# Optimization experiments

Measured on AMD Instinct MI355X. Metric: run time of the kernel, lower is better.

The kernel has to match this reference:

```python
import jax, jax.numpy as jnp
import numpy as np

LEVEL_SIZES = [256, 128, 64, 32, 16]  # FPN map sizes for a 1024x1024 image
B, N, C = 16, 64, 8
EPS = 1e-8


def setup_inputs() -> dict:
    key = jax.random.key(0)
    ks = jax.random.split(key, 9)
    inp = {}
    for l, s in enumerate(LEVEL_SIZES):
        # attention maps must be in (0,1) for binary_cross_entropy
        inp[f"attn{l}"] = jax.random.uniform(ks[l], (B, C, s, s), jnp.float32, 1e-4, 1.0 - 1e-4)
    # boxes: x1,y1 in-image; widths/heights in [8, 512] px so all levels get boxes
    x1 = jax.random.uniform(ks[5], (B, N)) * (1024.0 - 16.0)
    y1 = jax.random.uniform(ks[6], (B, N)) * (1024.0 - 16.0)
    dw = 8.0 + jax.random.uniform(ks[7], (B, N)) * 504.0
    dh = 8.0 + jax.random.uniform(ks[8], (B, N)) * 504.0
    x2 = jnp.minimum(x1 + dw, 1024.0)
    y2 = jnp.minimum(y1 + dh, 1024.0)
    inp["bboxs"] = jnp.stack([x1, y1, x2, y2], axis=-1)  # [B, N, 4]
    inp["img_h"] = 1024
    inp["img_w"] = 1024
    inp["alpha"] = 5
    inp["beta"] = 2
    return inp


def reference(attn0, attn1, attn2, attn3, attn4, bboxs, img_h, img_w, alpha, beta):
    attns = [attn0, attn1, attn2, attn3, attn4]
    h = float(img_h)
    w = float(img_w)
    x1, y1, x2, y2 = bboxs[..., 0], bboxs[..., 1], bboxs[..., 2], bboxs[..., 3]  # each [B, N]
    # original validity filter: coords <= image bounds
    valid = (x1 <= w) & (y1 <= h) & (x2 <= w) & (y2 <= h)  # [B, N]
    area = jnp.abs((x2 - x1) * (y2 - y1))  # [B, N]

    per_level = []  # list of [B, C] losses
    for l, a in enumerate(attns):
        _, _, Hl, Wl = a.shape
        side = 2.0 ** (l + alpha)
        min_a = side ** 2
        max_a = (side * beta) ** 2
        sel = valid & (area >= min_a) & (area <= max_a)  # [B, N]

        sx = Wl / w
        sy = Hl / h
        # integer pixel bounds: int() truncation == floor for nonneg coords, then clamp
        xi1 = jnp.maximum(jnp.floor(x1 * sx), 0.0)
        yi1 = jnp.maximum(jnp.floor(y1 * sy), 0.0)
        xi2 = jnp.minimum(jnp.ceil(x2 * sx) + 1.0, float(Wl))
        yi2 = jnp.minimum(jnp.ceil(y2 * sy) + 1.0, float(Hl))

        ys = jnp.arange(Hl, dtype=jnp.float32)
        xs = jnp.arange(Wl, dtype=jnp.float32)
        # separable per-box row/col indicators; fold the level selector into rows
        row = ((ys[None, None, :] >= yi1[..., None]) & (ys[None, None, :] < yi2[..., None])
               & sel[..., None]).astype(jnp.float32)  # [B, N, Hl]
        col = ((xs[None, None, :] >= xi1[..., None]) & (xs[None, None, :] < xi2[..., None])
               ).astype(jnp.float32)  # [B, N, Wl]
        # OR over boxes == (sum of outer products) > 0
        mask_gt = (jnp.einsum('bnh,bnw->bhw', row, col) > 0).astype(jnp.float32)  # [B, Hl, Wl]

        t = mask_gt[:, None, :, :]  # broadcast over channels
        p = a  # [B, C, Hl, Wl]
        bce = jnp.mean(-(t * jnp.log(p) + (1.0 - t) * jnp.log(1.0 - p)), axis=(2, 3))  # [B, C]
        inter = 2.0 * jnp.sum(p * t, axis=(2, 3)) + EPS
        union = jnp.sum(p, axis=(2, 3)) + jnp.sum(t, axis=(2, 3)) + EPS
        dice = 1.0 - inter / union  # [B, C]
        per_level.append(0.5 * bce + 0.5 * dice)

    losses = jnp.stack(per_level, axis=1)  # [B, L, C]
    per_image = losses.mean(axis=(1, 2))  # [B]
    has_box = valid.any(axis=1)
    per_image = jnp.where(has_box, per_image, 0.0)
    return per_image.mean(keepdims=True)  # shape [1]
```

## Files before the change

kernel.cpp:

```cpp
#include <hip/hip_runtime.h>
#include <cstdint>

#define NBOX 64
#define NB   16
#define NC   8


__device__ __forceinline__ unsigned long long range_mask(int a, int e, int base) {
    int lo = a - base; lo = lo < 0 ? 0 : (lo > 64 ? 64 : lo);
    int hi = e - base; hi = hi < 0 ? 0 : (hi > 64 ? 64 : hi);
    if (hi <= lo) return 0ULL;
    unsigned long long hm = (hi >= 64) ? ~0ULL : ((1ULL << hi) - 1ULL);
    unsigned long long lm = (1ULL << lo) - 1ULL;
    return hm & ~lm;
}

__global__ __launch_bounds__(256)
void k_mask(const float* __restrict__ bboxs,
            const int* __restrict__ ih_p, const int* __restrict__ iw_p,
            const int* __restrict__ alpha_p, const int* __restrict__ beta_p,
            unsigned long long* __restrict__ mask,
            float* __restrict__ tcnt) {
    const int bid = blockIdx.x;
    const int l = bid % 5, b = bid / 5;
    const int Hl = 256 >> l;
    const int W64 = (Hl >= 64) ? (Hl >> 6) : 1;
    const int mb_[5] = {0, 16384, 20480, 21504, 22016};
    const int mbase = mb_[l] + b * Hl * W64;

    const float w = (float)iw_p[0], h = (float)ih_p[0];
    const int alpha = alpha_p[0], beta = beta_p[0];
    const float side = (float)(1 << (l + alpha));
    const float min_a = side * side;
    const float sb = side * (float)beta;
    const float max_a = sb * sb;
    const float sx = (float)Hl / w;
    const float sy = (float)Hl / h;

    __shared__ int rx1[NBOX], rx2[NBOX], ry1[NBOX], ry2[NBOX];
    const int tid = threadIdx.x;
    if (tid < NBOX) {
        const float* bb = bboxs + (size_t)(b * NBOX + tid) * 4;
        float x1 = bb[0], y1 = bb[1], x2 = bb[2], y2 = bb[3];
        bool valid = (x1 <= w) && (y1 <= h) && (x2 <= w) && (y2 <= h);
        float area = fabsf((x2 - x1) * (y2 - y1));
        bool sel = valid && (area >= min_a) && (area <= max_a);
        int xi1 = (int)fmaxf(floorf(x1 * sx), 0.f);
        int yi1 = (int)fmaxf(floorf(y1 * sy), 0.f);
        int xi2 = (int)fminf(ceilf(x2 * sx) + 1.f, (float)Hl);
        int yi2 = (int)fminf(ceilf(y2 * sy) + 1.f, (float)Hl);
        rx1[tid] = xi1; rx2[tid] = xi2;
        ry1[tid] = sel ? yi1 : 0;
        ry2[tid] = sel ? yi2 : 0;
    }
    __syncthreads();

    int myt = 0;
    for (int hh = tid; hh < Hl; hh += 256) {
        unsigned long long m0 = 0, m1 = 0, m2 = 0, m3 = 0;
        for (int n = 0; n < NBOX; ++n) {
            if (hh >= ry1[n] && hh < ry2[n]) {
                int a = rx1[n], e = rx2[n];
                m0 |= range_mask(a, e, 0);
                m1 |= range_mask(a, e, 64);
                m2 |= range_mask(a, e, 128);
                m3 |= range_mask(a, e, 192);
            }
        }
        unsigned long long* dst = mask + mbase + hh * W64;
        dst[0] = m0;              myt += __popcll(m0);
        if (W64 > 1) { dst[1] = m1; myt += __popcll(m1); }
        if (W64 > 2) { dst[2] = m2; myt += __popcll(m2);
                       dst[3] = m3; myt += __popcll(m3); }
    }

    for (int off = 32; off > 0; off >>= 1) myt += __shfl_down(myt, off, 64);
    __shared__ int red[4];
    if ((tid & 63) == 0) red[tid >> 6] = myt;
    __syncthreads();
    if (tid == 0)
        tcnt[l * NB + b] = (float)(red[0] + red[1] + red[2] + red[3]);
}

__global__ __launch_bounds__(256)
void k_sums(const float* __restrict__ a0, const float* __restrict__ a1,
            const float* __restrict__ a2, const float* __restrict__ a3,
            const float* __restrict__ a4,
            const unsigned long long* __restrict__ mask,
            float* __restrict__ acc) {
    const int bid = blockIdx.x;
    int l, rel;
    if      (bid < 1024) { l = 0; rel = bid; }
    else if (bid < 1280) { l = 1; rel = bid - 1024; }
    else if (bid < 1408) { l = 2; rel = bid - 1280; }
    else if (bid < 1536) { l = 3; rel = bid - 1408; }
    else                 { l = 4; rel = bid - 1536; }
    const int ntl[5] = {8, 2, 1, 1, 1};
    const int mb_[5] = {0, 16384, 20480, 21504, 22016};
    const int nt = ntl[l];
    const int tile = rel % nt;
    const int bc = rel / nt;
    const int c = bc & 7, b = bc >> 3;
    const int Hl = 256 >> l;
    const int P  = Hl * Hl;
    const int logW = 8 - l;
    const int W64 = (Hl >= 64) ? (Hl >> 6) : 1;

    const float* attn = (l == 0) ? a0 : (l == 1) ? a1 : (l == 2) ? a2 : (l == 3) ? a3 : a4;
    const float* p = attn + (size_t)(b * NC + c) * P;
    const unsigned long long* mrow = mask + mb_[l] + b * Hl * W64;

    const int start = tile * 8192;
    const int end = min(start + 8192, P);

    float bce = 0.f, ps = 0.f, pts = 0.f;
    const int tid = threadIdx.x;
    for (int i = start + tid * 4; i < end; i += 1024) {
        float4 v = *(const float4*)(p + i);
        int hh = i >> logW;
        int ww = i & (Hl - 1);
        unsigned long long wd = mrow[hh * W64 + (ww >> 6)];
        unsigned int bits = (unsigned int)(wd >> (ww & 63)) & 0xFu;
        { float pv = v.x; bool t = bits & 1u; bce -= __logf(t ? pv : 1.f - pv); ps += pv; if (t) pts += pv; }
        { float pv = v.y; bool t = bits & 2u; bce -= __logf(t ? pv : 1.f - pv); ps += pv; if (t) pts += pv; }
        { float pv = v.z; bool t = bits & 4u; bce -= __logf(t ? pv : 1.f - pv); ps += pv; if (t) pts += pv; }
        { float pv = v.w; bool t = bits & 8u; bce -= __logf(t ? pv : 1.f - pv); ps += pv; if (t) pts += pv; }
    }

    for (int off = 32; off > 0; off >>= 1) {
        bce += __shfl_down(bce, off, 64);
        ps  += __shfl_down(ps,  off, 64);
        pts += __shfl_down(pts, off, 64);
    }
    __shared__ float red[4][3];
    if ((tid & 63) == 0) {
        int wv = tid >> 6;
        red[wv][0] = bce; red[wv][1] = ps; red[wv][2] = pts;
    }
    __syncthreads();
    if (tid == 0) {
        float rb = red[0][0] + red[1][0] + red[2][0] + red[3][0];
        float rp = red[0][1] + red[1][1] + red[2][1] + red[3][1];
        float rt = red[0][2] + red[1][2] + red[2][2] + red[3][2];
        float* dst = acc + ((size_t)(l * NB + b) * NC + c) * 3;
        atomicAdd(dst + 0, rb);
        atomicAdd(dst + 1, rp);
        atomicAdd(dst + 2, rt);
    }
}

__global__ void k_final(const float* __restrict__ acc, const float* __restrict__ tcnt,
                        const float* __restrict__ bboxs,
                        const int* __restrict__ ih_p, const int* __restrict__ iw_p,
                        float* __restrict__ out) {
    const int tid = threadIdx.x;
    __shared__ float per_img[NB];
    const float w = (float)iw_p[0], h = (float)ih_p[0];
    if (tid < NB) {
        const int b = tid;
        float s = 0.f;
        for (int l = 0; l < 5; ++l) {
            int Hl = 256 >> l;
            float invP = 1.f / (float)(Hl * Hl);
            float tc = tcnt[l * NB + b];
            for (int c = 0; c < NC; ++c) {
                const float* a = acc + ((size_t)(l * NB + b) * NC + c) * 3;
                float bce = a[0] * invP;
                float inter = 2.f * a[2] + 1e-8f;
                float uni = a[1] + tc + 1e-8f;
                float dice = 1.f - inter / uni;
                s += 0.5f * bce + 0.5f * dice;
            }
        }
        s *= (1.f / 40.f);
        bool has = false;
        const float* bb = bboxs + (size_t)b * NBOX * 4;
        for (int n = 0; n < NBOX; ++n) {
            float x1 = bb[n * 4 + 0], y1 = bb[n * 4 + 1];
            float x2 = bb[n * 4 + 2], y2 = bb[n * 4 + 3];
            if (x1 <= w && y1 <= h && x2 <= w && y2 <= h) { has = true; break; }
        }
        per_img[b] = has ? s : 0.f;
    }
    __syncthreads();
    if (tid == 0) {
        float t = 0.f;
        for (int i = 0; i < NB; ++i) t += per_img[i];
        out[0] = t * (1.f / (float)NB);
    }
}

extern "C" void kernel_launch(void* const* d_in, const int* in_sizes, int n_in,
                              void* d_out, int out_size, void* d_ws, size_t ws_size,
                              hipStream_t stream) {
    const float* a0 = (const float*)d_in[0];
    const float* a1 = (const float*)d_in[1];
    const float* a2 = (const float*)d_in[2];
    const float* a3 = (const float*)d_in[3];
    const float* a4 = (const float*)d_in[4];
    const float* bboxs = (const float*)d_in[5];
    const int* ih = (const int*)d_in[6];
    const int* iw = (const int*)d_in[7];
    const int* al = (const int*)d_in[8];
    const int* be = (const int*)d_in[9];

    float* acc = (float*)d_ws;
    float* tcnt = acc + 1920;
    unsigned long long* mask = (unsigned long long*)((char*)d_ws + 8192);

    hipMemsetAsync(d_ws, 0, 1920 * sizeof(float), stream);
    k_mask<<<80, 256, 0, stream>>>(bboxs, ih, iw, al, be, mask, tcnt);
    k_sums<<<1664, 256, 0, stream>>>(a0, a1, a2, a3, a4, mask, acc);
    k_final<<<1, 64, 0, stream>>>(acc, tcnt, bboxs, ih, iw, (float*)d_out);
}
```

Before: 118.9 us.

## Fuse mask building, reductions, and finalization into one kernel with last-block reduce

The separate mask, sums and final kernels are merged into a single kernel. Each block now computes the row bitmasks for its own tile into shared memory instead of reading a global mask. Per-block partials go to distinct slots and a counter-based last-block pattern performs the final reduction, which replaces the float atomics, the memset and two extra launches. The cost is redundant mask computation across channel and tile blocks, plus a serial tail in the last block.

```diff
diff --git a/kernel.cpp b/kernel.cpp
--- a/kernel.cpp
+++ b/kernel.cpp
@@ -4,6 +4,8 @@
 #define NBOX 64
 #define NB   16
 #define NC   8
+#define NBLK 1664
+#define EPSF 1e-8f
 
 
 __device__ __forceinline__ unsigned long long range_mask(int a, int e, int base) {
@@ -15,18 +17,35 @@
     return hm & ~lm;
 }
 
+__global__ void k_init(unsigned int* __restrict__ counter) {
+    if (threadIdx.x == 0) *counter = 0u;
+}
+
 __global__ __launch_bounds__(256)
-void k_mask(const float* __restrict__ bboxs,
+void k_main(const float* __restrict__ a0, const float* __restrict__ a1,
+            const float* __restrict__ a2, const float* __restrict__ a3,
+            const float* __restrict__ a4,
+            const float* __restrict__ bboxs,
             const int* __restrict__ ih_p, const int* __restrict__ iw_p,
             const int* __restrict__ alpha_p, const int* __restrict__ beta_p,
-            unsigned long long* __restrict__ mask,
-            float* __restrict__ tcnt) {
+            float* __restrict__ partials, unsigned int* __restrict__ counter,
+            float* __restrict__ out) {
     const int bid = blockIdx.x;
-    const int l = bid % 5, b = bid / 5;
+    int l, rel;
+    if      (bid < 1024) { l = 0; rel = bid; }
+    else if (bid < 1280) { l = 1; rel = bid - 1024; }
+    else if (bid < 1408) { l = 2; rel = bid - 1280; }
+    else if (bid < 1536) { l = 3; rel = bid - 1408; }
+    else                 { l = 4; rel = bid - 1536; }
+    const int ntl[5] = {8, 2, 1, 1, 1};
+    const int nt = ntl[l];
+    const int tile = rel % nt;
+    const int bc = rel / nt;
+    const int c = bc & 7, b = bc >> 3;
     const int Hl = 256 >> l;
+    const int P  = Hl * Hl;
+    const int logW = 8 - l;
     const int W64 = (Hl >= 64) ? (Hl >> 6) : 1;
-    const int mb_[5] = {0, 16384, 20480, 21504, 22016};
-    const int mbase = mb_[l] + b * Hl * W64;
 
     const float w = (float)iw_p[0], h = (float)ih_p[0];
     const int alpha = alpha_p[0], beta = beta_p[0];
@@ -38,25 +57,36 @@
     const float sy = (float)Hl / h;
 
     __shared__ int rx1[NBOX], rx2[NBOX], ry1[NBOX], ry2[NBOX];
+    __shared__ unsigned long long rowm[64][4];
+    __shared__ float redf[4][4];
+    __shared__ int last_flag;
+    __shared__ float pimg[NB];
+
     const int tid = threadIdx.x;
+
     if (tid < NBOX) {
         const float* bb = bboxs + (size_t)(b * NBOX + tid) * 4;
         float x1 = bb[0], y1 = bb[1], x2 = bb[2], y2 = bb[3];
         bool valid = (x1 <= w) && (y1 <= h) && (x2 <= w) && (y2 <= h);
         float area = fabsf((x2 - x1) * (y2 - y1));
         bool sel = valid && (area >= min_a) && (area <= max_a);
-        int xi1 = (int)fmaxf(floorf(x1 * sx), 0.f);
+        rx1[tid] = (int)fmaxf(floorf(x1 * sx), 0.f);
+        rx2[tid] = (int)fminf(ceilf(x2 * sx) + 1.f, (float)Hl);
         int yi1 = (int)fmaxf(floorf(y1 * sy), 0.f);
-        int xi2 = (int)fminf(ceilf(x2 * sx) + 1.f, (float)Hl);
         int yi2 = (int)fminf(ceilf(y2 * sy) + 1.f, (float)Hl);
-        rx1[tid] = xi1; rx2[tid] = xi2;
         ry1[tid] = sel ? yi1 : 0;
         ry2[tid] = sel ? yi2 : 0;
     }
     __syncthreads();
 
-    int myt = 0;
-    for (int hh = tid; hh < Hl; hh += 256) {
+    const int tpx = (P < 8192) ? P : 8192;
+    const int start = tile * 8192;
+    const int end = start + tpx;
+    const int r0 = start >> logW;
+    const int nrows = tpx >> logW;
+    float my_t = 0.f;
+    if (tid < nrows) {
+        const int hh = r0 + tid;
         unsigned long long m0 = 0, m1 = 0, m2 = 0, m3 = 0;
         for (int n = 0; n < NBOX; ++n) {
             if (hh >= ry1[n] && hh < ry2[n]) {
@@ -67,59 +97,23 @@
                 m3 |= range_mask(a, e, 192);
             }
         }
-        unsigned long long* dst = mask + mbase + hh * W64;
-        dst[0] = m0;              myt += __popcll(m0);
-        if (W64 > 1) { dst[1] = m1; myt += __popcll(m1); }
-        if (W64 > 2) { dst[2] = m2; myt += __popcll(m2);
-                       dst[3] = m3; myt += __popcll(m3); }
-    }
-
-    for (int off = 32; off > 0; off >>= 1) myt += __shfl_down(myt, off, 64);
-    __shared__ int red[4];
-    if ((tid & 63) == 0) red[tid >> 6] = myt;
-    __syncthreads();
-    if (tid == 0)
-        tcnt[l * NB + b] = (float)(red[0] + red[1] + red[2] + red[3]);
-}
-
-__global__ __launch_bounds__(256)
-void k_sums(const float* __restrict__ a0, const float* __restrict__ a1,
-            const float* __restrict__ a2, const float* __restrict__ a3,
-            const float* __restrict__ a4,
-            const unsigned long long* __restrict__ mask,
-            float* __restrict__ acc) {
-    const int bid = blockIdx.x;
-    int l, rel;
-    if      (bid < 1024) { l = 0; rel = bid; }
-    else if (bid < 1280) { l = 1; rel = bid - 1024; }
-    else if (bid < 1408) { l = 2; rel = bid - 1280; }
-    else if (bid < 1536) { l = 3; rel = bid - 1408; }
-    else                 { l = 4; rel = bid - 1536; }
-    const int ntl[5] = {8, 2, 1, 1, 1};
-    const int mb_[5] = {0, 16384, 20480, 21504, 22016};
-    const int nt = ntl[l];
-    const int tile = rel % nt;
-    const int bc = rel / nt;
-    const int c = bc & 7, b = bc >> 3;
-    const int Hl = 256 >> l;
-    const int P  = Hl * Hl;
-    const int logW = 8 - l;
-    const int W64 = (Hl >= 64) ? (Hl >> 6) : 1;
+        rowm[tid][0] = m0;
+        rowm[tid][1] = m1;
+        rowm[tid][2] = m2;
+        rowm[tid][3] = m3;
+        my_t = (float)(__popcll(m0) + __popcll(m1) + __popcll(m2) + __popcll(m3));
+    }
+    __syncthreads();
 
     const float* attn = (l == 0) ? a0 : (l == 1) ? a1 : (l == 2) ? a2 : (l == 3) ? a3 : a4;
     const float* p = attn + (size_t)(b * NC + c) * P;
-    const unsigned long long* mrow = mask + mb_[l] + b * Hl * W64;
-
-    const int start = tile * 8192;
-    const int end = min(start + 8192, P);
 
     float bce = 0.f, ps = 0.f, pts = 0.f;
-    const int tid = threadIdx.x;
     for (int i = start + tid * 4; i < end; i += 1024) {
         float4 v = *(const float4*)(p + i);
-        int hh = i >> logW;
+        int hr = (i >> logW) - r0;
         int ww = i & (Hl - 1);
-        unsigned long long wd = mrow[hh * W64 + (ww >> 6)];
+        unsigned long long wd = rowm[hr][ww >> 6];
         unsigned int bits = (unsigned int)(wd >> (ww & 63)) & 0xFu;
         { float pv = v.x; bool t = bits & 1u; bce -= __logf(t ? pv : 1.f - pv); ps += pv; if (t) pts += pv; }
         { float pv = v.y; bool t = bits & 2u; bce -= __logf(t ? pv : 1.f - pv); ps += pv; if (t) pts += pv; }
@@ -128,65 +122,69 @@
     }
 
     for (int off = 32; off > 0; off >>= 1) {
-        bce += __shfl_down(bce, off, 64);
-        ps  += __shfl_down(ps,  off, 64);
-        pts += __shfl_down(pts, off, 64);
-    }
-    __shared__ float red[4][3];
+        bce  += __shfl_down(bce,  off, 64);
+        ps   += __shfl_down(ps,   off, 64);
+        pts  += __shfl_down(pts,  off, 64);
+        my_t += __shfl_down(my_t, off, 64);
+    }
     if ((tid & 63) == 0) {
         int wv = tid >> 6;
-        red[wv][0] = bce; red[wv][1] = ps; red[wv][2] = pts;
+        redf[wv][0] = bce; redf[wv][1] = ps; redf[wv][2] = pts; redf[wv][3] = my_t;
     }
     __syncthreads();
     if (tid == 0) {
-        float rb = red[0][0] + red[1][0] + red[2][0] + red[3][0];
-        float rp = red[0][1] + red[1][1] + red[2][1] + red[3][1];
-        float rt = red[0][2] + red[1][2] + red[2][2] + red[3][2];
-        float* dst = acc + ((size_t)(l * NB + b) * NC + c) * 3;
-        atomicAdd(dst + 0, rb);
-        atomicAdd(dst + 1, rp);
-        atomicAdd(dst + 2, rt);
-    }
-}
-
-__global__ void k_final(const float* __restrict__ acc, const float* __restrict__ tcnt,
-                        const float* __restrict__ bboxs,
-                        const int* __restrict__ ih_p, const int* __restrict__ iw_p,
-                        float* __restrict__ out) {
-    const int tid = threadIdx.x;
-    __shared__ float per_img[NB];
-    const float w = (float)iw_p[0], h = (float)ih_p[0];
-    if (tid < NB) {
-        const int b = tid;
-        float s = 0.f;
-        for (int l = 0; l < 5; ++l) {
-            int Hl = 256 >> l;
-            float invP = 1.f / (float)(Hl * Hl);
-            float tc = tcnt[l * NB + b];
-            for (int c = 0; c < NC; ++c) {
-                const float* a = acc + ((size_t)(l * NB + b) * NC + c) * 3;
-                float bce = a[0] * invP;
-                float inter = 2.f * a[2] + 1e-8f;
-                float uni = a[1] + tc + 1e-8f;
-                float dice = 1.f - inter / uni;
-                s += 0.5f * bce + 0.5f * dice;
+        float* slot = partials + (size_t)bid * 4;
+        slot[0] = redf[0][0] + redf[1][0] + redf[2][0] + redf[3][0];
+        slot[1] = redf[0][1] + redf[1][1] + redf[2][1] + redf[3][1];
+        slot[2] = redf[0][2] + redf[1][2] + redf[2][2] + redf[3][2];
+        slot[3] = redf[0][3] + redf[1][3] + redf[2][3] + redf[3][3];
+        __threadfence();
+        unsigned int old = atomicAdd(counter, 1u);
+        last_flag = (old == NBLK - 1) ? 1 : 0;
+    }
+    __syncthreads();
+
+    if (last_flag) {
+        __threadfence();
+        if (tid < NB) pimg[tid] = 0.f;
+        __syncthreads();
+        const int lvl_base[5] = {0, 1024, 1280, 1408, 1536};
+        for (int combo = tid; combo < 640; combo += 256) {
+            int cl = combo >> 7;
+            int cbc = combo & 127;
+            int cnt = ntl[cl];
+            const float* s0 = partials + (size_t)(lvl_base[cl] + cbc * cnt) * 4;
+            float sb_ = 0.f, sp = 0.f, st = 0.f, sc = 0.f;
+            for (int t = 0; t < cnt; ++t) {
+                sb_ += s0[t * 4 + 0];
+                sp  += s0[t * 4 + 1];
+                st  += s0[t * 4 + 2];
+                sc  += s0[t * 4 + 3];
             }
-        }
-        s *= (1.f / 40.f);
-        bool has = false;
-        const float* bb = bboxs + (size_t)b * NBOX * 4;
-        for (int n = 0; n < NBOX; ++n) {
-            float x1 = bb[n * 4 + 0], y1 = bb[n * 4 + 1];
-            float x2 = bb[n * 4 + 2], y2 = bb[n * 4 + 3];
-            if (x1 <= w && y1 <= h && x2 <= w && y2 <= h) { has = true; break; }
-        }
-        per_img[b] = has ? s : 0.f;
-    }
-    __syncthreads();
-    if (tid == 0) {
-        float t = 0.f;
-        for (int i = 0; i < NB; ++i) t += per_img[i];
-        out[0] = t * (1.f / (float)NB);
+            int HH = 256 >> cl;
+            float invP = 1.f / (float)(HH * HH);
+            float dice = 1.f - (2.f * st + EPSF) / (sp + sc + EPSF);
+            float loss = 0.5f * sb_ * invP + 0.5f * dice;
+            atomicAdd(&pimg[cbc >> 3], loss);
+        }
+        __syncthreads();
+        if (tid < NB) {
+            const int bb_ = tid;
+            bool has = false;
+            const float* bb = bboxs + (size_t)bb_ * NBOX * 4;
+            for (int n = 0; n < NBOX; ++n) {
+                float x1 = bb[n * 4 + 0], y1 = bb[n * 4 + 1];
+                float x2 = bb[n * 4 + 2], y2 = bb[n * 4 + 3];
+                if (x1 <= w && y1 <= h && x2 <= w && y2 <= h) { has = true; break; }
+            }
+            pimg[bb_] = has ? pimg[bb_] * (1.f / 40.f) : 0.f;
+        }
+        __syncthreads();
+        if (tid == 0) {
+            float t = 0.f;
+            for (int i = 0; i < NB; ++i) t += pimg[i];
+            out[0] = t * (1.f / (float)NB);
+        }
     }
 }
 
@@ -204,12 +202,10 @@
     const int* al = (const int*)d_in[8];
     const int* be = (const int*)d_in[9];
 
-    float* acc = (float*)d_ws;
-    float* tcnt = acc + 1920;
-    unsigned long long* mask = (unsigned long long*)((char*)d_ws + 8192);
-
-    hipMemsetAsync(d_ws, 0, 1920 * sizeof(float), stream);
-    k_mask<<<80, 256, 0, stream>>>(bboxs, ih, iw, al, be, mask, tcnt);
-    k_sums<<<1664, 256, 0, stream>>>(a0, a1, a2, a3, a4, mask, acc);
-    k_final<<<1, 64, 0, stream>>>(acc, tcnt, bboxs, ih, iw, (float*)d_out);
-}
+    float* partials = (float*)d_ws;
+    unsigned int* counter = (unsigned int*)((char*)d_ws + NBLK * 4 * sizeof(float));
+
+    k_init<<<1, 64, 0, stream>>>(counter);
+    k_main<<<NBLK, 256, 0, stream>>>(a0, a1, a2, a3, a4, bboxs, ih, iw, al, be,
+                                     partials, counter, (float*)d_out);
+}
```

Measured after the change: 153.4 us. 1.29x slower.
